# Optimization experiments

Hardware: AMD Instinct MI355X
Metric: run time of the kernel (lower is better)

The kernel has to match this reference:

```python
import jax, jax.numpy as jnp
import numpy as np

H = 16  # n_heads (init kwarg)


def pos_enc(length, dim):
    # torch PositionalEncoding: pe[:,0::2]=sin, pe[:,1::2]=cos
    pos = jnp.arange(length, dtype=jnp.float32)[:, None]
    div = jnp.exp(jnp.arange(0, dim, 2, dtype=jnp.float32) * (-np.log(10000.0) / dim))
    ang = pos * div  # [L, dim/2]
    return jnp.stack([jnp.sin(ang), jnp.cos(ang)], axis=-1).reshape(length, dim)


def torch_ln(x, a, b, eps=1e-6):
    # custom LayerNorm: a*(x-mean)/(std+eps)+b with unbiased std (torch default)
    mean = x.mean(-1, keepdims=True)
    n = x.shape[-1]
    var = ((x - mean) ** 2).sum(-1, keepdims=True) / (n - 1)
    return a * (x - mean) / (jnp.sqrt(var) + eps) + b


def setup_inputs() -> dict:
    key = jax.random.key(0)
    ks = jax.random.split(key, 16)
    B, Lq, Lk, qd, kd, hid, mid = 8, 512, 1024, 768, 768, 1024, 4096
    s = 0.02  # weight init scale
    w = lambda k, shape: jax.random.normal(k, shape, jnp.float32) * s
    return dict(
        q=jax.random.normal(ks[0], (B, Lq, qd), jnp.float32),
        k=jax.random.normal(ks[1], (B, Lk, kd), jnp.float32),
        Wq=w(ks[2], (qd, hid)), bq=jnp.zeros(hid, jnp.float32),
        Wk=w(ks[3], (kd, hid)), bk=jnp.zeros(hid, jnp.float32),
        Wv=w(ks[4], (kd, hid)), bv=jnp.zeros(hid, jnp.float32),
        Wv0=w(ks[5], (kd, hid)), bv0=jnp.zeros(hid, jnp.float32),
        Wq0=w(ks[6], (qd, hid)), bq0=jnp.zeros(hid, jnp.float32),
        nq_a=jnp.ones(hid, jnp.float32), nq_b=jnp.zeros(hid, jnp.float32),
        nx_a=jnp.ones(hid, jnp.float32), nx_b=jnp.zeros(hid, jnp.float32),
        W1=w(ks[7], (hid, mid)), b1=jnp.zeros(mid, jnp.float32),
        W2=w(ks[8], (mid, hid)), b2=jnp.zeros(hid, jnp.float32),
        ns_a=jnp.ones(hid, jnp.float32), ns_b=jnp.zeros(hid, jnp.float32),
    )


def reference(q, k, Wq, bq, Wk, bk, Wv, bv, Wv0, bv0, Wq0, bq0,
              nq_a, nq_b, nx_a, nx_b, W1, b1, W2, b2, ns_a, ns_b):
    # FocalAtt(mode='CA').forward(q, k, PE='qk', SF=True, outmode='atted_bilinear')
    B, Lq, qd = q.shape
    Lk, kd = k.shape[1], k.shape[2]
    hid = Wq.shape[1]
    dh = hid // H
    q0 = q
    qp = q + pos_enc(Lq, qd)  # PosEnc_q (dropout=0)
    kp = k + pos_enc(Lk, kd)  # PosEnc_k
    # AttM: manual multi-head scores
    qh = (qp @ Wq + bq).reshape(B, Lq, H, dh).transpose(0, 2, 1, 3)  # bhqd
    kh = (kp @ Wk + bk).reshape(B, Lk, H, dh).transpose(0, 2, 1, 3)  # bhkd
    scores = jnp.einsum('bhqd,bhkd->bhqk', qh, kh) / jnp.sqrt(jnp.float32(dh))
    att = jax.nn.softmax(scores, axis=-1)  # SF=True
    q0p = q0 @ Wq0 + bq0  # [B, Lq, hid]
    # 'atted' branch
    v1 = (kp @ Wv + bv).reshape(B, Lk, H, dh).transpose(0, 2, 1, 3)
    atted = jnp.einsum('bhqk,bhkd->bhqd', att, v1)
    atted = atted.transpose(0, 2, 1, 3).reshape(B, Lq, hid)
    atted = torch_ln(q0p + atted, nq_a, nq_b)
    # 'bilinear' branch: einsum('bhvk,bhvq,bhqk->bhk')
    q0h = q0p.reshape(B, Lq, H, dh).transpose(0, 2, 1, 3)  # bhvd, v=Lq
    v0 = (kp @ Wv0 + bv0).reshape(B, Lk, H, dh).transpose(0, 2, 1, 3)  # bhqd, q=Lk
    x = jnp.einsum('bhvd,bhvq,bhqd->bhd', q0h, att, v0).reshape(B, hid)
    x = torch_ln(x, nx_a, nx_b)
    # attention output: relu over scores, mean over heads
    att_out = jax.nn.relu(scores).sum(axis=1) / jnp.float32(H)  # [B, Lq, Lk]
    # SorCA: FFN + residual + LayerNorm
    ff = jax.nn.relu(atted @ W1 + b1) @ W2 + b2
    qq = torch_ln(atted + ff, ns_a, ns_b)
    # FocalAtt returns (feature, q, k, attention, attidx_q, attidx_k); drop Nones
    return (x, qq, kp, att_out)
```

## Files before the change

### kernel.cpp

```cpp
#include <hip/hip_runtime.h>


typedef unsigned short bfr;
using short8 = __attribute__((ext_vector_type(8))) short;
using f32x4  = __attribute__((ext_vector_type(4))) float;

__device__ __forceinline__ float b2f(bfr s) {
  return __uint_as_float(((unsigned int)s) << 16);
}
__device__ __forceinline__ bfr f2b(float f) {
  unsigned int u = __float_as_uint(f);
  u += 0x7fffu + ((u >> 16) & 1u);
  return (bfr)(u >> 16);
}

struct __align__(8) us4 { bfr x, y, z, w; };

__device__ __forceinline__ float4 load4f(const float* p) { return *(const float4*)p; }
__device__ __forceinline__ float4 load4f(const bfr* p) {
  us4 u = *(const us4*)p;
  return make_float4(b2f(u.x), b2f(u.y), b2f(u.z), b2f(u.w));
}
__device__ __forceinline__ void store4(float* p, float a, float b, float c, float d) {
  *(float4*)p = make_float4(a, b, c, d);
}
__device__ __forceinline__ void store4(bfr* p, float a, float b, float c, float d) {
  us4 v; v.x = f2b(a); v.y = f2b(b); v.z = f2b(c); v.w = f2b(d);
  *(us4*)p = v;
}

__device__ __forceinline__ void gll16(const bfr* g, bfr* l) {
  __builtin_amdgcn_global_load_lds(
      (const __attribute__((address_space(1))) unsigned int*)g,
      (__attribute__((address_space(3))) unsigned int*)l, 16, 0, 0);
}

__device__ __forceinline__ float pe_val(int l, int d) {
  float ang = (float)l * expf((float)(d & ~1) * (-9.210340371976184f / 768.0f));
  return (d & 1) ? cosf(ang) : sinf(ang);
}

__global__ __launch_bounds__(256) void posenc_k(const float* __restrict__ in,
                                                float* __restrict__ outf,
                                                bfr* __restrict__ outb, int total) {
  int idx = blockIdx.x * 256 + threadIdx.x;
  if (idx >= total) return;
  float v = in[idx] + pe_val((idx / 768) % 1024, idx % 768);
  outf[idx] = v;
  outb[idx] = f2b(v);
}

__global__ __launch_bounds__(256) void posenc_q_all(const float* __restrict__ in,
                                                    bfr* __restrict__ out,
                                                    bfr* __restrict__ outraw,
                                                    int total) {
  int idx = blockIdx.x * 256 + threadIdx.x;
  if (idx >= total) return;
  float v = in[idx];
  out[idx] = f2b(v + pe_val((idx / 768) % 512, idx % 768));
  outraw[idx] = f2b(v);
}

__global__ __launch_bounds__(256) void transpose_w(const float* __restrict__ src,
                                                   bfr* __restrict__ dst,
                                                   int rows, int cols, int ld,
                                                   int mode) {
  __shared__ float t[32][33];
  const int bc = blockIdx.x * 32, br = blockIdx.y * 32;
  const int tx = threadIdx.x & 31, ty = threadIdx.x >> 5;
#pragma unroll
  for (int i = 0; i < 4; i++)
    t[ty + i * 8][tx] = src[(size_t)(br + ty + i * 8) * ld + bc + tx];
  __syncthreads();
#pragma unroll
  for (int i = 0; i < 4; i++) {
    int c = bc + ty + i * 8;
    int r = (mode == 0) ? c : ((c >> 6) * 128 + (c & 63) + (mode == 2 ? 64 : 0));
    dst[(size_t)r * rows + br + tx] = f2b(t[tx][ty + i * 8]);
  }
}

template <typename TC>
__device__ __forceinline__ void mgemm_body(const bfr* __restrict__ A,
                                           const bfr* __restrict__ BT,
                                           const float* __restrict__ bias,
                                           TC* __restrict__ C,
                                           int K, int ldc, int relu, int accum,
                                           int m0, int n0,
                                           bfr* __restrict__ As,
                                           bfr* __restrict__ Bs) {
  const int tid = threadIdx.x;
  const int lane = tid & 63, w = tid >> 6;
  const int wm = (w & 1) * 64, wn = (w >> 1) * 64;
  const int grow = w * 32 + (lane >> 3);
  const int gkc = (lane & 7) * 8;
  const int fr = lane & 15, fc = (lane >> 4) * 8;
  const int NT = K >> 6;
  f32x4 acc[4][4];
#pragma unroll
  for (int i = 0; i < 4; i++)
#pragma unroll
    for (int j = 0; j < 4; j++) acc[i][j] = (f32x4){0.f, 0.f, 0.f, 0.f};

  auto issue = [&](int t, int buf) {
    const int k0 = t << 6;
    const bfr* Ag = A + (size_t)(m0 + grow) * K + k0 + gkc;
    const bfr* Bg = BT + (size_t)(n0 + grow) * K + k0 + gkc;
#pragma unroll
    for (int i = 0; i < 4; i++)
      gll16(Ag + (size_t)(i * 8) * K, As + buf * 8192 + (w * 32 + i * 8) * 64);
#pragma unroll
    for (int i = 0; i < 4; i++)
      gll16(Bg + (size_t)(i * 8) * K, Bs + buf * 8192 + (w * 32 + i * 8) * 64);
  };

  issue(0, 0);
  __syncthreads();
  int cur = 0;
  for (int t = 0; t < NT; ++t) {
    const bool more = (t + 1 < NT);
    if (more) issue(t + 1, cur ^ 1);
#pragma unroll
    for (int ks = 0; ks < 2; ks++) {
      short8 af[4], bf4[4];
#pragma unroll
      for (int i = 0; i < 4; i++)
        af[i] = *(const short8*)(As + cur * 8192 + (wm + i * 16 + fr) * 64 + ks * 32 + fc);
#pragma unroll
      for (int i = 0; i < 4; i++)
        bf4[i] = *(const short8*)(Bs + cur * 8192 + (wn + i * 16 + fr) * 64 + ks * 32 + fc);
#pragma unroll
      for (int i = 0; i < 4; i++)
#pragma unroll
        for (int j = 0; j < 4; j++)
          acc[i][j] = __builtin_amdgcn_mfma_f32_16x16x32_bf16(af[i], bf4[j], acc[i][j], 0, 0, 0);
    }
    if (more) {
      __syncthreads();
      cur ^= 1;
    }
  }
  const int col0 = n0 + wn + fr;
  const int row0 = m0 + wm + (lane >> 4) * 4;
  float bsv[4];
#pragma unroll
  for (int j = 0; j < 4; j++) bsv[j] = bias ? bias[col0 + j * 16] : 0.f;
#pragma unroll
  for (int i = 0; i < 4; i++) {
#pragma unroll
    for (int j = 0; j < 4; j++) {
      const int col = col0 + j * 16;
#pragma unroll
      for (int r = 0; r < 4; r++) {
        const int row = row0 + i * 16 + r;
        float v = acc[i][j][r] + bsv[j];
        if (relu) v = fmaxf(v, 0.f);
        size_t idx = (size_t)row * ldc + col;
        if constexpr (sizeof(TC) == 2) {
          C[idx] = f2b(v);
        } else {
          if (accum) C[idx] += v; else C[idx] = v;
        }
      }
    }
  }
}

template <typename TC>
__global__ __launch_bounds__(256) void mgemm(const bfr* __restrict__ A,
                                             const bfr* __restrict__ BT,
                                             const float* __restrict__ bias,
                                             TC* __restrict__ C,
                                             int K, int ldc, int relu, int accum) {
  __shared__ bfr As[2][8192];
  __shared__ bfr Bs[2][8192];
  const int nwg = gridDim.x * gridDim.y;
  const int bid = blockIdx.y * gridDim.x + blockIdx.x;
  const int q8 = nwg >> 3, r8 = nwg & 7;
  const int xcd = bid & 7, off = bid >> 3;
  const int swz = (xcd < r8 ? xcd * (q8 + 1) : r8 * (q8 + 1) + (xcd - r8) * q8) + off;
  const int n0 = (swz % gridDim.x) * 128, m0 = (swz / gridDim.x) * 128;
  mgemm_body<TC>(A, BT, bias, C, K, ldc, relu, accum, m0, n0,
                 &As[0][0], &Bs[0][0]);
}

__global__ __launch_bounds__(256) void kv_gemm(const bfr* __restrict__ kp16,
                                               const bfr* __restrict__ WkT,
                                               const float* __restrict__ bk,
                                               bfr* __restrict__ kh,
                                               const bfr* __restrict__ WTvv,
                                               bfr* __restrict__ vT) {
  __shared__ bfr As[2][8192];
  __shared__ bfr Bs[2][8192];
  const int swz = (blockIdx.x & 7) * 24 + (blockIdx.x >> 3);
  if (swz < 64) {
    mgemm_body<bfr>(kp16, WkT, bk, kh, 768, 1024, 0, 0,
                    (swz >> 3) * 128, (swz & 7) * 128, &As[0][0], &Bs[0][0]);
  } else {
    const int s = swz - 64;
    mgemm_body<bfr>(WTvv, kp16, nullptr, vT, 768, 1024, 0, 0,
                    (s >> 3) * 128, (s & 7) * 128, &As[0][0], &Bs[0][0]);
  }
}

__global__ __launch_bounds__(256) void proj_gemm(const bfr* __restrict__ q16,
                                                 const bfr* __restrict__ Wq0T,
                                                 const float* __restrict__ bq0,
                                                 bfr* __restrict__ q0p,
                                                 const bfr* __restrict__ qp_all,
                                                 const bfr* __restrict__ WqT,
                                                 const float* __restrict__ bq,
                                                 bfr* __restrict__ qh) {
  __shared__ bfr As[2][8192];
  __shared__ bfr Bs[2][8192];
  const int swz = (blockIdx.x & 7) * 64 + (blockIdx.x >> 3);
  if (swz < 256) {
    mgemm_body<bfr>(q16, Wq0T, bq0, q0p, 768, 1024, 0, 0,
                    (swz >> 3) * 128, (swz & 7) * 128, &As[0][0], &Bs[0][0]);
  } else {
    const int s = swz - 256;
    mgemm_body<bfr>(qp_all, WqT, bq, qh, 768, 1024, 0, 0,
                    (s >> 3) * 128, (s & 7) * 128, &As[0][0], &Bs[0][0]);
  }
}

__global__ __launch_bounds__(256) void score_mfma(const bfr* __restrict__ qh,
                                                  const bfr* __restrict__ kh,
                                                  bfr* __restrict__ sc) {
  __shared__ __align__(16) bfr Qs[128][72];
  __shared__ __align__(16) bfr Ks[128][72];
  const int h = blockIdx.z, q0 = blockIdx.y * 128, k0 = blockIdx.x * 128;
  const int tid = threadIdx.x, lane = tid & 63;
  const int wm = ((tid >> 6) & 1) * 64, wn = (tid >> 7) * 64;
  const int fr = lane & 15, fc = (lane >> 4) * 8;
  {
    const int r = tid >> 1, c = (tid & 1) * 32;
    const bfr* qsrc = qh + (size_t)(q0 + r) * 1024 + h * 64 + c;
    const bfr* ksrc = kh + (size_t)(k0 + r) * 1024 + h * 64 + c;
#pragma unroll
    for (int i = 0; i < 4; i++) {
      *(short8*)&Qs[r][c + i * 8] = *(const short8*)(qsrc + i * 8);
      *(short8*)&Ks[r][c + i * 8] = *(const short8*)(ksrc + i * 8);
    }
  }
  __syncthreads();
  f32x4 acc[4][4];
#pragma unroll
  for (int i = 0; i < 4; i++)
#pragma unroll
    for (int j = 0; j < 4; j++) acc[i][j] = (f32x4){0.f, 0.f, 0.f, 0.f};
#pragma unroll
  for (int ks = 0; ks < 2; ks++) {
    short8 af[4], bf[4];
#pragma unroll
    for (int t = 0; t < 4; t++) af[t] = *(const short8*)&Qs[wm + t * 16 + fr][ks * 32 + fc];
#pragma unroll
    for (int t = 0; t < 4; t++) bf[t] = *(const short8*)&Ks[wn + t * 16 + fr][ks * 32 + fc];
#pragma unroll
    for (int i = 0; i < 4; i++)
#pragma unroll
      for (int j = 0; j < 4; j++)
        acc[i][j] = __builtin_amdgcn_mfma_f32_16x16x32_bf16(af[i], bf[j], acc[i][j], 0, 0, 0);
  }
  const int col0 = k0 + wn + fr;
  const int row0 = q0 + wm + (lane >> 4) * 4;
#pragma unroll
  for (int i = 0; i < 4; i++)
#pragma unroll
    for (int j = 0; j < 4; j++)
#pragma unroll
      for (int r = 0; r < 4; r++)
        sc[((size_t)h * 512 + row0 + i * 16 + r) * 1024 + col0 + j * 16] =
            f2b(acc[i][j][r] * 0.125f);
}

__global__ __launch_bounds__(256) void smax_ao(bfr* __restrict__ sc,
                                               float* __restrict__ ao) {
  __shared__ float part[4][1024];
  const int q = blockIdx.x;
  const int tid = threadIdx.x, lane = tid & 63, w = tid >> 6;
  float aos[16];
#pragma unroll
  for (int i = 0; i < 16; i++) aos[i] = 0.f;
#pragma unroll
  for (int i = 0; i < 4; i++) {
    const int h = w * 4 + i;
    bfr* row = sc + ((size_t)h * 512 + q) * 1024 + lane * 16;
    us4 raw[4];
    float v[16];
#pragma unroll
    for (int j = 0; j < 4; j++) raw[j] = ((const us4*)row)[j];
#pragma unroll
    for (int j = 0; j < 4; j++) {
      v[j * 4 + 0] = b2f(raw[j].x); v[j * 4 + 1] = b2f(raw[j].y);
      v[j * 4 + 2] = b2f(raw[j].z); v[j * 4 + 3] = b2f(raw[j].w);
    }
    float m = v[0];
#pragma unroll
    for (int j = 1; j < 16; j++) m = fmaxf(m, v[j]);
#pragma unroll
    for (int j = 0; j < 16; j++) aos[j] += fmaxf(v[j], 0.f);
    for (int o = 32; o; o >>= 1) m = fmaxf(m, __shfl_xor(m, o, 64));
    float s = 0.f;
#pragma unroll
    for (int j = 0; j < 16; j++) { v[j] = expf(v[j] - m); s += v[j]; }
    for (int o = 32; o; o >>= 1) s += __shfl_xor(s, o, 64);
    const float inv = 1.0f / s;
#pragma unroll
    for (int j = 0; j < 4; j++) {
      raw[j].x = f2b(v[j * 4 + 0] * inv); raw[j].y = f2b(v[j * 4 + 1] * inv);
      raw[j].z = f2b(v[j * 4 + 2] * inv); raw[j].w = f2b(v[j * 4 + 3] * inv);
      ((us4*)row)[j] = raw[j];
    }
  }
#pragma unroll
  for (int j = 0; j < 4; j++)
    *(float4*)&part[w][lane * 16 + j * 4] =
        make_float4(aos[j * 4], aos[j * 4 + 1], aos[j * 4 + 2], aos[j * 4 + 3]);
  __syncthreads();
  const int k4 = tid * 4;
  float4 a0 = *(const float4*)&part[0][k4];
  float4 a1 = *(const float4*)&part[1][k4];
  float4 a2 = *(const float4*)&part[2][k4];
  float4 a3 = *(const float4*)&part[3][k4];
  store4(ao + (size_t)q * 1024 + k4,
         (a0.x + a1.x + a2.x + a3.x) * 0.0625f, (a0.y + a1.y + a2.y + a3.y) * 0.0625f,
         (a0.z + a1.z + a2.z + a3.z) * 0.0625f, (a0.w + a1.w + a2.w + a3.w) * 0.0625f);
}

__global__ __launch_bounds__(256) void attv2(const bfr* __restrict__ att,
                                             const bfr* __restrict__ vT,
                                             const float* __restrict__ bv,
                                             const float* __restrict__ bv0,
                                             bfr* __restrict__ atp,
                                             bfr* __restrict__ u) {
  __shared__ __align__(16) bfr As[32][72];
  __shared__ __align__(16) bfr Bs[128][72];
  const int h = blockIdx.y, q0 = blockIdx.x * 32;
  const int tid = threadIdx.x, lane = tid & 63, w = tid >> 6;
  const int fr = lane & 15, fc = (lane >> 4) * 8;
  const int wm = (w & 1) * 16, wn = (w >> 1) * 64;
  const bfr* attb = att + ((size_t)h * 512 + q0) * 1024;
  const bfr* vb = vT + (size_t)h * 128 * 1024;
  const int ar = tid >> 3, ac = (tid & 7) * 8;
  const int br = tid >> 2, bc = (tid & 3) * 16;
  f32x4 acc[4];
#pragma unroll
  for (int t = 0; t < 4; t++) acc[t] = (f32x4){0.f, 0.f, 0.f, 0.f};
  for (int k0 = 0; k0 < 1024; k0 += 64) {
    *(short8*)&As[ar][ac] = *(const short8*)(attb + (size_t)ar * 1024 + k0 + ac);
    *(short8*)&Bs[br][bc] = *(const short8*)(vb + (size_t)br * 1024 + k0 + bc);
    *(short8*)&Bs[br][bc + 8] = *(const short8*)(vb + (size_t)br * 1024 + k0 + bc + 8);
    *(short8*)&Bs[br + 64][bc] = *(const short8*)(vb + (size_t)(br + 64) * 1024 + k0 + bc);
    *(short8*)&Bs[br + 64][bc + 8] =
        *(const short8*)(vb + (size_t)(br + 64) * 1024 + k0 + bc + 8);
    __syncthreads();
#pragma unroll
    for (int ks = 0; ks < 2; ks++) {
      short8 af = *(const short8*)&As[wm + fr][ks * 32 + fc];
#pragma unroll
      for (int t = 0; t < 4; t++) {
        short8 bf = *(const short8*)&Bs[wn + t * 16 + fr][ks * 32 + fc];
        acc[t] = __builtin_amdgcn_mfma_f32_16x16x32_bf16(af, bf, acc[t], 0, 0, 0);
      }
    }
    __syncthreads();
  }
  const int row0 = q0 + wm + (lane >> 4) * 4;
  bfr* o = (wn == 0) ? atp : u;
  const float* bias = (wn == 0) ? bv : bv0;
#pragma unroll
  for (int t = 0; t < 4; t++) {
    const int cm = t * 16 + fr;
    const float bb = bias[h * 64 + cm];
#pragma unroll
    for (int r = 0; r < 4; r++)
      o[(size_t)(row0 + r) * 1024 + h * 64 + cm] = f2b(acc[t][r] + bb);
  }
}

__global__ __launch_bounds__(256) void xpre_kernel(const bfr* __restrict__ q0p,
                                                   const bfr* __restrict__ u,
                                                   float* __restrict__ xpre) {
  const int c = blockIdx.x * 256 + threadIdx.x;
  const int r0 = blockIdx.y * 64;
  const bfr* qp = q0p + (size_t)r0 * 1024 + c;
  const bfr* up = u + (size_t)r0 * 1024 + c;
  float s = 0.f;
#pragma unroll 8
  for (int r = 0; r < 64; r++)
    s = fmaf(b2f(qp[(size_t)r * 1024]), b2f(up[(size_t)r * 1024]), s);
  atomicAdd(&xpre[c], s);
}

template <typename TX, typename TY, typename OT>
__global__ __launch_bounds__(256) void ln_kernel(const TX* __restrict__ X,
                                                 const TY* __restrict__ Y,
                                                 const float* __restrict__ ga,
                                                 const float* __restrict__ be,
                                                 OT* __restrict__ out) {
  __shared__ float sm[4];
  const size_t row = blockIdx.x;
  const int tid = threadIdx.x;
  float4 v = load4f(X + row * 1024 + tid * 4);
  if (Y) {
    float4 w = load4f(Y + row * 1024 + tid * 4);
    v.x += w.x; v.y += w.y; v.z += w.z; v.w += w.w;
  }
  float s = v.x + v.y + v.z + v.w;
  for (int o = 32; o; o >>= 1) s += __shfl_down(s, o, 64);
  if ((tid & 63) == 0) sm[tid >> 6] = s;
  __syncthreads();
  s = sm[0] + sm[1] + sm[2] + sm[3];
  float mean = s * (1.0f / 1024.0f);
  float d0 = v.x - mean, d1 = v.y - mean, d2 = v.z - mean, d3 = v.w - mean;
  float q = d0 * d0 + d1 * d1 + d2 * d2 + d3 * d3;
  __syncthreads();
  for (int o = 32; o; o >>= 1) q += __shfl_down(q, o, 64);
  if ((tid & 63) == 0) sm[tid >> 6] = q;
  __syncthreads();
  q = sm[0] + sm[1] + sm[2] + sm[3];
  float rs = 1.0f / (sqrtf(q * (1.0f / 1023.0f)) + 1e-6f);
  float4 g = *(const float4*)(ga + tid * 4);
  float4 bb = *(const float4*)(be + tid * 4);
  store4(out + row * 1024 + tid * 4,
         g.x * d0 * rs + bb.x, g.y * d1 * rs + bb.y,
         g.z * d2 * rs + bb.z, g.w * d3 * rs + bb.w);
}

extern "C" void kernel_launch(void* const* d_in, const int* in_sizes, int n_in,
                              void* d_out, int out_size, void* d_ws, size_t ws_size,
                              hipStream_t stream) {
  (void)in_sizes; (void)n_in; (void)out_size; (void)ws_size;
  const float* q   = (const float*)d_in[0];
  const float* k   = (const float*)d_in[1];
  const float* Wq  = (const float*)d_in[2];
  const float* bq  = (const float*)d_in[3];
  const float* Wk  = (const float*)d_in[4];
  const float* bk  = (const float*)d_in[5];
  const float* Wv  = (const float*)d_in[6];
  const float* bv  = (const float*)d_in[7];
  const float* Wv0 = (const float*)d_in[8];
  const float* bv0 = (const float*)d_in[9];
  const float* Wq0 = (const float*)d_in[10];
  const float* bq0 = (const float*)d_in[11];
  const float* nqa = (const float*)d_in[12];
  const float* nqb = (const float*)d_in[13];
  const float* nxa = (const float*)d_in[14];
  const float* nxb = (const float*)d_in[15];
  const float* W1  = (const float*)d_in[16];
  const float* b1  = (const float*)d_in[17];
  const float* W2  = (const float*)d_in[18];
  const float* b2  = (const float*)d_in[19];
  const float* nsa = (const float*)d_in[20];
  const float* nsb = (const float*)d_in[21];

  float* out = (float*)d_out;
  float* x_out  = out;
  float* qq_out = out + 8192;
  float* kp_out = out + 4202496;
  float* ao_out = out + 10493952;
  bfr* kp16 = (bfr*)qq_out;

  char* base = (char*)d_ws;
  bfr* q0p   = (bfr*)(base + 0);
  bfr* qh    = (bfr*)(base + 8388608);
  bfr* atl   = (bfr*)(base + 16777216);
  bfr* WqT   = (bfr*)(base + 25165824);
  bfr* Wq0T  = (bfr*)(base + 26738688);
  bfr* WTkv  = (bfr*)(base + 28311552);
  float* xpre = (float*)(base + 33030144);
  char* S = base + 33062912;
  bfr* sc    = (bfr*)(S + 0);
  bfr* vT    = (bfr*)(S + 16777216);
  bfr* atpb  = (bfr*)(S + 20971520);
  bfr* ub    = (bfr*)(S + 22020096);
  bfr* kh    = (bfr*)(S + 23068672);
  bfr* qp_all = (bfr*)(S + 0);
  bfr* q16    = (bfr*)(S + 6291456);
  bfr* W1Tn  = (bfr*)(S + 0);
  bfr* W2Tn  = (bfr*)(S + 4194304);
  bfr* ff1n  = (bfr*)(S + 8388608);
  float* ff2a = (float*)(base + 0);

  posenc_k<<<24576, 256, 0, stream>>>(k, kp_out, kp16, 6291456);
  posenc_q_all<<<12288, 256, 0, stream>>>(q, qp_all, q16, 3145728);
  transpose_w<<<dim3(32, 24), 256, 0, stream>>>(Wq, WqT, 768, 1024, 1024, 0);
  transpose_w<<<dim3(32, 24), 256, 0, stream>>>(Wq0, Wq0T, 768, 1024, 1024, 0);
  transpose_w<<<dim3(32, 24), 256, 0, stream>>>(Wk, WTkv, 768, 1024, 1024, 0);
  transpose_w<<<dim3(32, 24), 256, 0, stream>>>(Wv, WTkv + 786432, 768, 1024, 1024, 1);
  transpose_w<<<dim3(32, 24), 256, 0, stream>>>(Wv0, WTkv + 786432, 768, 1024, 1024, 2);

  proj_gemm<<<512, 256, 0, stream>>>(q16, Wq0T, bq0, q0p, qp_all, WqT, bq, qh);
  hipMemsetAsync(xpre, 0, 32768, stream);

  for (int b = 0; b < 8; b++) {
    const bfr* kp_b = kp16 + (size_t)b * 786432;
    kv_gemm<<<192, 256, 0, stream>>>(kp_b, WTkv, bk, kh, WTkv + 786432, vT);
    score_mfma<<<dim3(8, 4, 16), 256, 0, stream>>>(qh + (size_t)b * 524288, kh, sc);
    smax_ao<<<512, 256, 0, stream>>>(sc, ao_out + (size_t)b * 524288);
    attv2<<<dim3(16, 16), 256, 0, stream>>>(sc, vT, bv, bv0, atpb, ub);
    xpre_kernel<<<dim3(4, 8), 256, 0, stream>>>(q0p + (size_t)b * 524288, ub,
                                                xpre + b * 1024);
    ln_kernel<bfr, bfr, bfr><<<512, 256, 0, stream>>>(
        q0p + (size_t)b * 524288, atpb, nqa, nqb, atl + (size_t)b * 524288);
  }

  ln_kernel<float, float, float><<<8, 256, 0, stream>>>(xpre, (const float*)nullptr,
                                                        nxa, nxb, x_out);

  for (int nc = 0; nc < 2; nc++) {
    transpose_w<<<dim3(64, 32), 256, 0, stream>>>(W1 + nc * 2048, W1Tn,
                                                  1024, 2048, 4096, 0);
    transpose_w<<<dim3(32, 64), 256, 0, stream>>>(W2 + (size_t)nc * 2048 * 1024, W2Tn,
                                                  2048, 1024, 1024, 0);
    mgemm<bfr><<<dim3(16, 32), 256, 0, stream>>>(
        atl, W1Tn, b1 + nc * 2048, ff1n, 1024, 2048, 1, 0);
    mgemm<float><<<dim3(8, 32), 256, 0, stream>>>(
        ff1n, W2Tn, nc == 0 ? b2 : nullptr, ff2a, 2048, 1024, 0, nc);
  }
  ln_kernel<bfr, float, float><<<4096, 256, 0, stream>>>(atl, ff2a, nsa, nsb, qq_out);
}
```

Baseline: 846.1 us.

## Batch KV projection over two batches, add 128x64 GEMM tiles, async attv2 loads

Adds a 128x64-tile GEMM variant and uses it for the second FFN GEMM and for a new K/V projection kernel that covers two batches per launch, so each launch has more workgroups to fill the GPU. The attention-times-V kernel switches to double-buffered direct-to-LDS global loads with one barrier per K tile. It also raises wave priority around the MFMA loops via s_setprio. The trade-offs are more workspace juggling (vT1 is aliased into the output buffer), smaller tiles that reuse less data, and the risk of buffer aliasing errors.

```diff
diff --git a/kernel.cpp b/kernel.cpp
--- a/kernel.cpp
+++ b/kernel.cpp
@@ -120,6 +120,7 @@
   for (int t = 0; t < NT; ++t) {
     const bool more = (t + 1 < NT);
     if (more) issue(t + 1, cur ^ 1);
+    __builtin_amdgcn_s_setprio(1);
 #pragma unroll
     for (int ks = 0; ks < 2; ks++) {
       short8 af[4], bf4[4];
@@ -135,6 +136,7 @@
         for (int j = 0; j < 4; j++)
           acc[i][j] = __builtin_amdgcn_mfma_f32_16x16x32_bf16(af[i], bf4[j], acc[i][j], 0, 0, 0);
     }
+    __builtin_amdgcn_s_setprio(0);
     if (more) {
       __syncthreads();
       cur ^= 1;
@@ -149,6 +151,93 @@
   for (int i = 0; i < 4; i++) {
 #pragma unroll
     for (int j = 0; j < 4; j++) {
+      const int col = col0 + j * 16;
+#pragma unroll
+      for (int r = 0; r < 4; r++) {
+        const int row = row0 + i * 16 + r;
+        float v = acc[i][j][r] + bsv[j];
+        if (relu) v = fmaxf(v, 0.f);
+        size_t idx = (size_t)row * ldc + col;
+        if constexpr (sizeof(TC) == 2) {
+          C[idx] = f2b(v);
+        } else {
+          if (accum) C[idx] += v; else C[idx] = v;
+        }
+      }
+    }
+  }
+}
+
+template <typename TC>
+__device__ __forceinline__ void mgemm_body64(const bfr* __restrict__ A,
+                                             const bfr* __restrict__ BT,
+                                             const float* __restrict__ bias,
+                                             TC* __restrict__ C,
+                                             int K, int ldc, int relu, int accum,
+                                             int m0, int n0,
+                                             bfr* __restrict__ As,
+                                             bfr* __restrict__ Bs) {
+  const int tid = threadIdx.x;
+  const int lane = tid & 63, w = tid >> 6;
+  const int wm = (w & 1) * 64, wn = (w >> 1) * 32;
+  const int grow = lane >> 3, gkc = (lane & 7) * 8;
+  const int fr = lane & 15, fc = (lane >> 4) * 8;
+  const int NT = K >> 6;
+  f32x4 acc[4][2];
+#pragma unroll
+  for (int i = 0; i < 4; i++)
+#pragma unroll
+    for (int j = 0; j < 2; j++) acc[i][j] = (f32x4){0.f, 0.f, 0.f, 0.f};
+
+  auto issue = [&](int t, int buf) {
+    const int k0 = t << 6;
+    const bfr* Ag = A + (size_t)(m0 + w * 32 + grow) * K + k0 + gkc;
+#pragma unroll
+    for (int i = 0; i < 4; i++)
+      gll16(Ag + (size_t)(i * 8) * K, As + buf * 8192 + (w * 32 + i * 8) * 64);
+    const bfr* Bg = BT + (size_t)(n0 + w * 16 + grow) * K + k0 + gkc;
+#pragma unroll
+    for (int i = 0; i < 2; i++)
+      gll16(Bg + (size_t)(i * 8) * K, Bs + buf * 4096 + (w * 16 + i * 8) * 64);
+  };
+
+  issue(0, 0);
+  __syncthreads();
+  int cur = 0;
+  for (int t = 0; t < NT; ++t) {
+    const bool more = (t + 1 < NT);
+    if (more) issue(t + 1, cur ^ 1);
+    __builtin_amdgcn_s_setprio(1);
+#pragma unroll
+    for (int ks = 0; ks < 2; ks++) {
+      short8 af[4], bf4[2];
+#pragma unroll
+      for (int i = 0; i < 4; i++)
+        af[i] = *(const short8*)(As + cur * 8192 + (wm + i * 16 + fr) * 64 + ks * 32 + fc);
+#pragma unroll
+      for (int j = 0; j < 2; j++)
+        bf4[j] = *(const short8*)(Bs + cur * 4096 + (wn + j * 16 + fr) * 64 + ks * 32 + fc);
+#pragma unroll
+      for (int i = 0; i < 4; i++)
+#pragma unroll
+        for (int j = 0; j < 2; j++)
+          acc[i][j] = __builtin_amdgcn_mfma_f32_16x16x32_bf16(af[i], bf4[j], acc[i][j], 0, 0, 0);
+    }
+    __builtin_amdgcn_s_setprio(0);
+    if (more) {
+      __syncthreads();
+      cur ^= 1;
+    }
+  }
+  const int col0 = n0 + wn + fr;
+  const int row0 = m0 + wm + (lane >> 4) * 4;
+  float bsv[2];
+#pragma unroll
+  for (int j = 0; j < 2; j++) bsv[j] = bias ? bias[col0 + j * 16] : 0.f;
+#pragma unroll
+  for (int i = 0; i < 4; i++) {
+#pragma unroll
+    for (int j = 0; j < 2; j++) {
       const int col = col0 + j * 16;
 #pragma unroll
       for (int r = 0; r < 4; r++) {
@@ -184,22 +273,51 @@
                  &As[0][0], &Bs[0][0]);
 }
 
-__global__ __launch_bounds__(256) void kv_gemm(const bfr* __restrict__ kp16,
-                                               const bfr* __restrict__ WkT,
-                                               const float* __restrict__ bk,
-                                               bfr* __restrict__ kh,
-                                               const bfr* __restrict__ WTvv,
-                                               bfr* __restrict__ vT) {
+template <typename TC>
+__global__ __launch_bounds__(256) void mgemm64(const bfr* __restrict__ A,
+                                               const bfr* __restrict__ BT,
+                                               const float* __restrict__ bias,
+                                               TC* __restrict__ C,
+                                               int K, int ldc, int relu, int accum) {
   __shared__ bfr As[2][8192];
-  __shared__ bfr Bs[2][8192];
-  const int swz = (blockIdx.x & 7) * 24 + (blockIdx.x >> 3);
-  if (swz < 64) {
-    mgemm_body<bfr>(kp16, WkT, bk, kh, 768, 1024, 0, 0,
-                    (swz >> 3) * 128, (swz & 7) * 128, &As[0][0], &Bs[0][0]);
+  __shared__ bfr Bs[2][4096];
+  const int nwg = gridDim.x * gridDim.y;
+  const int bid = blockIdx.y * gridDim.x + blockIdx.x;
+  const int q8 = nwg >> 3, r8 = nwg & 7;
+  const int xcd = bid & 7, off = bid >> 3;
+  const int swz = (xcd < r8 ? xcd * (q8 + 1) : r8 * (q8 + 1) + (xcd - r8) * q8) + off;
+  const int n0 = (swz % gridDim.x) * 64, m0 = (swz / gridDim.x) * 128;
+  mgemm_body64<TC>(A, BT, bias, C, K, ldc, relu, accum, m0, n0,
+                   &As[0][0], &Bs[0][0]);
+}
+
+__global__ __launch_bounds__(256) void kv_gemm2(const bfr* __restrict__ kp0,
+                                                const bfr* __restrict__ kp1,
+                                                const bfr* __restrict__ WkT,
+                                                const float* __restrict__ bk,
+                                                bfr* __restrict__ kh0,
+                                                bfr* __restrict__ kh1,
+                                                const bfr* __restrict__ WTvv,
+                                                bfr* __restrict__ vT0,
+                                                bfr* __restrict__ vT1) {
+  __shared__ bfr As[2][8192];
+  __shared__ bfr Bs[2][4096];
+  const int swz = (blockIdx.x & 7) * 96 + (blockIdx.x >> 3);
+  if (swz < 128) {
+    mgemm_body64<bfr>(kp0, WkT, bk, kh0, 768, 1024, 0, 0,
+                      (swz >> 4) * 128, (swz & 15) * 64, &As[0][0], &Bs[0][0]);
+  } else if (swz < 256) {
+    const int s = swz - 128;
+    mgemm_body64<bfr>(kp1, WkT, bk, kh1, 768, 1024, 0, 0,
+                      (s >> 4) * 128, (s & 15) * 64, &As[0][0], &Bs[0][0]);
+  } else if (swz < 512) {
+    const int s = swz - 256;
+    mgemm_body64<bfr>(WTvv, kp0, nullptr, vT0, 768, 1024, 0, 0,
+                      (s >> 4) * 128, (s & 15) * 64, &As[0][0], &Bs[0][0]);
   } else {
-    const int s = swz - 64;
-    mgemm_body<bfr>(WTvv, kp16, nullptr, vT, 768, 1024, 0, 0,
-                    (s >> 3) * 128, (s & 7) * 128, &As[0][0], &Bs[0][0]);
+    const int s = swz - 512;
+    mgemm_body64<bfr>(WTvv, kp1, nullptr, vT1, 768, 1024, 0, 0,
+                      (s >> 4) * 128, (s & 15) * 64, &As[0][0], &Bs[0][0]);
   }
 }
 
@@ -249,6 +367,7 @@
   for (int i = 0; i < 4; i++)
 #pragma unroll
     for (int j = 0; j < 4; j++) acc[i][j] = (f32x4){0.f, 0.f, 0.f, 0.f};
+  __builtin_amdgcn_s_setprio(1);
 #pragma unroll
   for (int ks = 0; ks < 2; ks++) {
     short8 af[4], bf[4];
@@ -262,6 +381,7 @@
       for (int j = 0; j < 4; j++)
         acc[i][j] = __builtin_amdgcn_mfma_f32_16x16x32_bf16(af[i], bf[j], acc[i][j], 0, 0, 0);
   }
+  __builtin_amdgcn_s_setprio(0);
   const int col0 = k0 + wn + fr;
   const int row0 = q0 + wm + (lane >> 4) * 4;
 #pragma unroll
@@ -334,37 +454,49 @@
                                              const float* __restrict__ bv0,
                                              bfr* __restrict__ atp,
                                              bfr* __restrict__ u) {
-  __shared__ __align__(16) bfr As[32][72];
-  __shared__ __align__(16) bfr Bs[128][72];
+  __shared__ bfr As[2][32 * 64];
+  __shared__ bfr Bs[2][128 * 64];
   const int h = blockIdx.y, q0 = blockIdx.x * 32;
   const int tid = threadIdx.x, lane = tid & 63, w = tid >> 6;
   const int fr = lane & 15, fc = (lane >> 4) * 8;
   const int wm = (w & 1) * 16, wn = (w >> 1) * 64;
   const bfr* attb = att + ((size_t)h * 512 + q0) * 1024;
   const bfr* vb = vT + (size_t)h * 128 * 1024;
-  const int ar = tid >> 3, ac = (tid & 7) * 8;
-  const int br = tid >> 2, bc = (tid & 3) * 16;
+  const int grow = lane >> 3, gkc = (lane & 7) * 8;
   f32x4 acc[4];
 #pragma unroll
   for (int t = 0; t < 4; t++) acc[t] = (f32x4){0.f, 0.f, 0.f, 0.f};
-  for (int k0 = 0; k0 < 1024; k0 += 64) {
-    *(short8*)&As[ar][ac] = *(const short8*)(attb + (size_t)ar * 1024 + k0 + ac);
-    *(short8*)&Bs[br][bc] = *(const short8*)(vb + (size_t)br * 1024 + k0 + bc);
-    *(short8*)&Bs[br][bc + 8] = *(const short8*)(vb + (size_t)br * 1024 + k0 + bc + 8);
-    *(short8*)&Bs[br + 64][bc] = *(const short8*)(vb + (size_t)(br + 64) * 1024 + k0 + bc);
-    *(short8*)&Bs[br + 64][bc + 8] =
-        *(const short8*)(vb + (size_t)(br + 64) * 1024 + k0 + bc + 8);
-    __syncthreads();
+
+  auto issue = [&](int t, int buf) {
+    const int k0 = t << 6;
+    gll16(attb + (size_t)(w * 8 + grow) * 1024 + k0 + gkc, &As[buf][(w * 8) * 64]);
+#pragma unroll
+    for (int i = 0; i < 4; i++)
+      gll16(vb + (size_t)(w * 32 + i * 8 + grow) * 1024 + k0 + gkc,
+            &Bs[buf][(w * 32 + i * 8) * 64]);
+  };
+
+  issue(0, 0);
+  __syncthreads();
+  int cur = 0;
+  for (int t = 0; t < 16; ++t) {
+    const bool more = (t + 1 < 16);
+    if (more) issue(t + 1, cur ^ 1);
+    __builtin_amdgcn_s_setprio(1);
 #pragma unroll
     for (int ks = 0; ks < 2; ks++) {
-      short8 af = *(const short8*)&As[wm + fr][ks * 32 + fc];
-#pragma unroll
-      for (int t = 0; t < 4; t++) {
-        short8 bf = *(const short8*)&Bs[wn + t * 16 + fr][ks * 32 + fc];
-        acc[t] = __builtin_amdgcn_mfma_f32_16x16x32_bf16(af, bf, acc[t], 0, 0, 0);
+      short8 af = *(const short8*)&As[cur][(wm + fr) * 64 + ks * 32 + fc];
+#pragma unroll
+      for (int j = 0; j < 4; j++) {
+        short8 bf = *(const short8*)&Bs[cur][(wn + j * 16 + fr) * 64 + ks * 32 + fc];
+        acc[j] = __builtin_amdgcn_mfma_f32_16x16x32_bf16(af, bf, acc[j], 0, 0, 0);
       }
     }
-    __syncthreads();
+    __builtin_amdgcn_s_setprio(0);
+    if (more) {
+      __syncthreads();
+      cur ^= 1;
+    }
   }
   const int row0 = q0 + wm + (lane >> 4) * 4;
   bfr* o = (wn == 0) ? atp : u;
@@ -461,6 +593,7 @@
   float* kp_out = out + 4202496;
   float* ao_out = out + 10493952;
   bfr* kp16 = (bfr*)qq_out;
+  bfr* vT1  = kp16 + 6291456;
 
   char* base = (char*)d_ws;
   bfr* q0p   = (bfr*)(base + 0);
@@ -472,10 +605,13 @@
   float* xpre = (float*)(base + 33030144);
   char* S = base + 33062912;
   bfr* sc    = (bfr*)(S + 0);
-  bfr* vT    = (bfr*)(S + 16777216);
-  bfr* atpb  = (bfr*)(S + 20971520);
-  bfr* ub    = (bfr*)(S + 22020096);
-  bfr* kh    = (bfr*)(S + 23068672);
+  bfr* kh0   = (bfr*)(S + 16777216);
+  bfr* kh1   = (bfr*)(S + 18874368);
+  bfr* vT0   = (bfr*)(S + 20971520);
+  bfr* atp0  = (bfr*)(S + 16777216);
+  bfr* ub0   = (bfr*)(S + 17825792);
+  bfr* atp1  = (bfr*)(S + 18874368);
+  bfr* ub1   = (bfr*)(S + 19922944);
   bfr* qp_all = (bfr*)(S + 0);
   bfr* q16    = (bfr*)(S + 6291456);
   bfr* W1Tn  = (bfr*)(S + 0);
@@ -494,16 +630,26 @@
   proj_gemm<<<512, 256, 0, stream>>>(q16, Wq0T, bq0, q0p, qp_all, WqT, bq, qh);
   hipMemsetAsync(xpre, 0, 32768, stream);
 
-  for (int b = 0; b < 8; b++) {
-    const bfr* kp_b = kp16 + (size_t)b * 786432;
-    kv_gemm<<<192, 256, 0, stream>>>(kp_b, WTkv, bk, kh, WTkv + 786432, vT);
-    score_mfma<<<dim3(8, 4, 16), 256, 0, stream>>>(qh + (size_t)b * 524288, kh, sc);
-    smax_ao<<<512, 256, 0, stream>>>(sc, ao_out + (size_t)b * 524288);
-    attv2<<<dim3(16, 16), 256, 0, stream>>>(sc, vT, bv, bv0, atpb, ub);
-    xpre_kernel<<<dim3(4, 8), 256, 0, stream>>>(q0p + (size_t)b * 524288, ub,
-                                                xpre + b * 1024);
-    ln_kernel<bfr, bfr, bfr><<<512, 256, 0, stream>>>(
-        q0p + (size_t)b * 524288, atpb, nqa, nqb, atl + (size_t)b * 524288);
+  for (int p = 0; p < 4; p++) {
+    const int b0 = 2 * p, b1 = 2 * p + 1;
+    kv_gemm2<<<768, 256, 0, stream>>>(kp16 + (size_t)b0 * 786432,
+                                      kp16 + (size_t)b1 * 786432,
+                                      WTkv, bk, kh0, kh1,
+                                      WTkv + 786432, vT0, vT1);
+    for (int j = 0; j < 2; j++) {
+      const int b = b0 + j;
+      bfr* kh = j ? kh1 : kh0;
+      bfr* vT = j ? vT1 : vT0;
+      bfr* atpb = j ? atp1 : atp0;
+      bfr* ub = j ? ub1 : ub0;
+      score_mfma<<<dim3(8, 4, 16), 256, 0, stream>>>(qh + (size_t)b * 524288, kh, sc);
+      smax_ao<<<512, 256, 0, stream>>>(sc, ao_out + (size_t)b * 524288);
+      attv2<<<dim3(16, 16), 256, 0, stream>>>(sc, vT, bv, bv0, atpb, ub);
+      xpre_kernel<<<dim3(4, 8), 256, 0, stream>>>(q0p + (size_t)b * 524288, ub,
+                                                  xpre + b * 1024);
+      ln_kernel<bfr, bfr, bfr><<<512, 256, 0, stream>>>(
+          q0p + (size_t)b * 524288, atpb, nqa, nqb, atl + (size_t)b * 524288);
+    }
   }
 
   ln_kernel<float, float, float><<<8, 256, 0, stream>>>(xpre, (const float*)nullptr,
@@ -516,7 +662,7 @@
                                                   2048, 1024, 1024, 0);
     mgemm<bfr><<<dim3(16, 32), 256, 0, stream>>>(
         atl, W1Tn, b1 + nc * 2048, ff1n, 1024, 2048, 1, 0);
-    mgemm<float><<<dim3(8, 32), 256, 0, stream>>>(
+    mgemm64<float><<<dim3(16, 32), 256, 0, stream>>>(
         ff1n, W2Tn, nc == 0 ? b2 : nullptr, ff2a, 2048, 1024, 0, nc);
   }
   ln_kernel<bfr, float, float><<<4096, 256, 0, stream>>>(atl, ff2a, nsa, nsb, qq_out);
```

New measurement: 801.1 us. 5.3% less time.
